# Kernel tuning notes

Measured on AMD Instinct MI355X. Metric: run time of the kernel, lower is better.

The kernel has to match this reference:

```python
import jax, jax.numpy as jnp
import numpy as np

B, N, DIM, QK_DIM, HEADS, GS, M = 4, 8000, 256, 128, 8, 128, 256


def setup_inputs() -> dict:
    key = jax.random.key(0)
    ks = jax.random.split(key, 8)
    normed_x = jax.random.normal(ks[0], (B, N, DIM), jnp.float32)
    # idx_last is a per-batch permutation (token reordering index), shape [B, N, 1]
    idx_last = jax.vmap(lambda k: jax.random.permutation(k, N))(
        jax.random.split(ks[1], B)).astype(jnp.int32)[..., None]
    k_global = jax.random.normal(ks[2], (HEADS, M, QK_DIM // HEADS), jnp.float32)
    v_global = jax.random.normal(ks[3], (HEADS, M, DIM // HEADS), jnp.float32)
    s = 1.0 / np.sqrt(DIM).astype(np.float32)
    Wq = jax.random.normal(ks[4], (QK_DIM, DIM), jnp.float32) * s
    Wk = jax.random.normal(ks[5], (QK_DIM, DIM), jnp.float32) * s
    Wv = jax.random.normal(ks[6], (DIM, DIM), jnp.float32) * s
    Wp = jax.random.normal(ks[7], (DIM, DIM), jnp.float32) * s
    return {"normed_x": normed_x, "idx_last": idx_last, "k_global": k_global,
            "v_global": v_global, "Wq": Wq, "Wk": Wk, "Wv": Wv, "Wp": Wp}


def _forward(normed_x, idx_last, k_global, v_global, Wq, Wk, Wv, Wp):
    x = normed_x
    b, n, _ = x.shape
    h = HEADS
    idx = idx_last[..., 0]  # [B, N]

    q = x @ Wq.T  # [B, N, QK_DIM]
    k = x @ Wk.T  # [B, N, QK_DIM]
    v = x @ Wv.T  # [B, N, DIM]

    # reorder tokens (gather along the token axis)
    q = jnp.take_along_axis(q, idx[:, :, None], axis=1)
    k = jnp.take_along_axis(k, idx[:, :, None], axis=1)
    v = jnp.take_along_axis(v, idx[:, :, None], axis=1)

    gs = min(n, GS)
    ng = (n + gs - 1) // gs
    pad_n = ng * gs - n

    # pad queries by reflecting the tail, then split into ng groups of gs
    pq = jnp.concatenate([q, jnp.flip(q[:, n - pad_n:n], axis=1)], axis=1)
    pq = pq.reshape(b, ng, gs, h, -1).transpose(0, 1, 3, 2, 4)  # b ng h gs dq

    # keys/values padded with an extra gs of reflected tail -> overlapping windows
    kr = jnp.concatenate([k, jnp.flip(k[:, n - pad_n - gs:n], axis=1)], axis=1)
    vr = jnp.concatenate([v, jnp.flip(v[:, n - pad_n - gs:n], axis=1)], axis=1)
    k_win = jnp.concatenate([kr[:, :ng * gs].reshape(b, ng, gs, -1),
                             kr[:, gs:].reshape(b, ng, gs, -1)], axis=2)
    v_win = jnp.concatenate([vr[:, :ng * gs].reshape(b, ng, gs, -1),
                             vr[:, gs:].reshape(b, ng, gs, -1)], axis=2)
    pk = k_win.reshape(b, ng, 2 * gs, h, -1).transpose(0, 1, 3, 2, 4)  # b ng h 2gs dq
    pv = v_win.reshape(b, ng, 2 * gs, h, -1).transpose(0, 1, 3, 2, 4)  # b ng h 2gs dv

    scale = pq.shape[-1] ** (-0.5)

    # local overlapping-window attention
    s1 = jnp.einsum('bghqd,bghkd->bghqk', pq, pk) * scale
    o1 = jnp.einsum('bghqk,bghkd->bghqd', jax.nn.softmax(s1, axis=-1), pv)

    # global attention (k_global/v_global broadcast over batch and groups)
    s2 = jnp.einsum('bghqd,hmd->bghqm', pq, k_global) * scale
    o2 = jnp.einsum('bghqm,hmd->bghqd', jax.nn.softmax(s2, axis=-1), v_global)

    out = (o1 + o2).transpose(0, 1, 3, 2, 4).reshape(b, ng * gs, -1)[:, :n]

    # scatter back to original token order: res[b, idx[b, i]] = out[b, i]
    b_idx = jnp.arange(b)[:, None]
    out = out.at[b_idx, idx].set(out)
    return out @ Wp.T


def reference(normed_x, idx_last, k_global, v_global, Wq, Wk, Wv, Wp):
    return _forward(normed_x, idx_last, k_global, v_global, Wq, Wk, Wv, Wp)
```

## Files before the change

kernel.cpp:

```cpp
#include <hip/hip_runtime.h>

typedef __attribute__((ext_vector_type(8))) short short8;
typedef __attribute__((ext_vector_type(4))) short short4v;
typedef __attribute__((ext_vector_type(4))) float f32x4;
typedef unsigned short ushort_t;

#define MFMA_BF16_K32(A,B,C) __builtin_amdgcn_mfma_f32_16x16x32_bf16(A,B,C,0,0,0)
#define MFMA_BF16_K16(A,B,C) __builtin_amdgcn_mfma_f32_16x16x16bf16_1k(A,B,C,0,0,0)

static constexpr int Bc  = 4;
static constexpr int Nn  = 8000;
static constexpr int N2  = 8192;
static constexpr int DIMc = 256;
static constexpr float SC2 = 0.36067376022224085f;

__device__ __forceinline__ unsigned short f2bf(float f){
  unsigned int u = __float_as_uint(f);
  u = (u + 0x7FFFu + ((u >> 16) & 1u)) >> 16;
  return (unsigned short)u;
}
__device__ __forceinline__ uint2 pack4(f32x4 v){
  uint2 r;
  r.x = (unsigned)f2bf(v[0]) | ((unsigned)f2bf(v[1]) << 16);
  r.y = (unsigned)f2bf(v[2]) | ((unsigned)f2bf(v[3]) << 16);
  return r;
}
__device__ __forceinline__ unsigned cvtpk(float lo, float hi){
  unsigned r;
  asm("v_cvt_pk_bf16_f32 %0, %1, %2" : "=v"(r) : "v"(lo), "v"(hi));
  return r;
}
__device__ __forceinline__ float rexp2(float x){
  float r;
  asm("v_exp_f32 %0, %1" : "=v"(r) : "v"(x));
  return r;
}
__device__ __forceinline__ float bfhi(unsigned u){ return __uint_as_float(u & 0xffff0000u); }
__device__ __forceinline__ float bflo(unsigned u){ return __uint_as_float(u << 16); }
__device__ __forceinline__ int vperm(int t){
  return (t & ~31) | (((t >> 2) & 3) * 8 + ((t >> 4) & 1) * 4 + (t & 3));
}

__global__ __launch_bounds__(256) void prep_kernel(
    const float* __restrict__ Wq, const float* __restrict__ Wk,
    const float* __restrict__ Wv, const float* __restrict__ Wp,
    const float* __restrict__ kg, const float* __restrict__ vg,
    ushort_t* __restrict__ Wcs, ushort_t* __restrict__ Wps,
    ushort_t* __restrict__ vgT, ushort_t* __restrict__ kgb)
{
  int i = blockIdx.x * 256 + threadIdx.x;
  if (i < 131072){
    int jj = i & 7, f = i >> 3;
    int l = f & 63, kc = (f >> 6) & 7, ctw = f >> 9;
    int col = ctw * 16 + (l & 15);
    int k   = kc * 32 + (l >> 4) * 8 + jj;
    float v;
    if (col < 128)      v = Wq[col * 256 + k] * SC2;
    else if (col < 256) v = Wk[(col - 128) * 256 + k];
    else                v = Wv[(col - 256) * 256 + k];
    Wcs[i] = f2bf(v);
  } else if (i < 196608){
    int o = i - 131072;
    int jj = o & 7, f = o >> 3;
    int l = f & 63, kc = (f >> 6) & 7, ctw = f >> 9;
    int col = ctw * 16 + (l & 15);
    int k   = kc * 32 + (l >> 4) * 8 + jj;
    Wps[o] = f2bf(Wp[col * 256 + k]);
  } else if (i < 262144){
    int o = i - 196608;
    int c = o & 31, m = (o >> 5) & 255, h = o >> 13;
    vgT[(h * 32 + c) * 256 + vperm(m)] = f2bf(vg[o]);
  } else {
    int j = i - 262144;
    kgb[j] = f2bf(kg[j]);
  }
}

__global__ __launch_bounds__(256) void proj_kernel(
    const float* __restrict__ X, const ushort_t* __restrict__ Wcs,
    const int* __restrict__ idx, ushort_t* __restrict__ qh,
    ushort_t* __restrict__ kh, ushort_t* __restrict__ vT)
{
  const int b  = blockIdx.y;
  const int r0 = blockIdx.x * 64;
  const int tid = threadIdx.x;
  const int w = tid >> 6, l = tid & 63, g4 = l >> 4, q16 = l & 15;
  __shared__ unsigned Xs[64][132];

  #pragma unroll
  for (int r = 0; r < 16; ++r){
    int row = r * 4 + w;
    int tok = idx[b * Nn + r0 + row];
    float4 xv = reinterpret_cast<const float4*>(X + (size_t)(b * Nn + tok) * DIMc)[l];
    uint2 u; u.x = cvtpk(xv.x, xv.y); u.y = cvtpk(xv.z, xv.w);
    *reinterpret_cast<uint2*>(&Xs[row][l * 2]) = u;
  }
  __syncthreads();

  f32x4 acc[4][8];
  #pragma unroll
  for (int mt = 0; mt < 4; ++mt)
    #pragma unroll
    for (int ct = 0; ct < 8; ++ct) acc[mt][ct] = f32x4{0.f, 0.f, 0.f, 0.f};
  #pragma unroll
  for (int kc = 0; kc < 8; ++kc){
    short8 a[4];
    #pragma unroll
    for (int mt = 0; mt < 4; ++mt){
      uint4 au = *reinterpret_cast<const uint4*>(&Xs[mt * 16 + q16][kc * 16 + g4 * 4]);
      a[mt] = __builtin_bit_cast(short8, au);
    }
    #pragma unroll
    for (int ct = 0; ct < 8; ++ct){
      short8 bb = *reinterpret_cast<const short8*>(
          Wcs + ((size_t)((w * 8 + ct) * 8 + kc) * 64 + l) * 8);
      #pragma unroll
      for (int mt = 0; mt < 4; ++mt) acc[mt][ct] = MFMA_BF16_K32(a[mt], bb, acc[mt][ct]);
    }
  }
  if (w < 2){
    ushort_t* dst = (w == 0) ? qh : kh;
    #pragma unroll
    for (int ct = 0; ct < 8; ++ct){
      #pragma unroll
      for (int mt = 0; mt < 4; ++mt){
        #pragma unroll
        for (int r = 0; r < 4; ++r){
          int j = r0 + mt * 16 + g4 * 4 + r;
          dst[((size_t)(b * 8 + ct) * N2 + j) * 16 + q16] = f2bf(acc[mt][ct][r]);
        }
      }
    }
  } else {
    #pragma unroll
    for (int ct = 0; ct < 8; ++ct){
      int col = (w - 2) * 128 + ct * 16 + q16;
      #pragma unroll
      for (int mt = 0; mt < 4; ++mt){
        int jb = r0 + (mt >> 1) * 32 + g4 * 8 + (mt & 1) * 4;
        *reinterpret_cast<uint2*>(vT + (size_t)(b * 256 + col) * N2 + jb) = pack4(acc[mt][ct]);
      }
    }
  }
}

__global__ __launch_bounds__(256) void reflect_fill_kernel(
    ushort_t* __restrict__ qh, ushort_t* __restrict__ kh, ushort_t* __restrict__ vT)
{
  int t = blockIdx.x * 256 + threadIdx.x;
  if (t < 24576){
    int e = t & 1;
    int r = (t >> 1) % 192;
    int p = (t >> 1) / 192;
    int b = p >> 4, q = p & 15;
    ushort_t* base = (q < 8) ? qh : kh;
    int h = q & 7;
    size_t plane = (size_t)(b * 8 + h) * N2 * 16;
    const uint4* src = reinterpret_cast<const uint4*>(base + plane + (size_t)(7999 - r) * 16);
    uint4*       dst = reinterpret_cast<uint4*>(base + plane + (size_t)(8000 + r) * 16);
    dst[e] = src[e];
  } else {
    int u = t - 24576;
    int r = u / 192, i2 = u % 192;
    vT[(size_t)r * N2 + vperm(8000 + i2)] = vT[(size_t)r * N2 + vperm(7999 - i2)];
  }
}

__global__ __launch_bounds__(256) void attn_kernel(
    const ushort_t* __restrict__ qh, const ushort_t* __restrict__ kh,
    const ushort_t* __restrict__ vT,
    const ushort_t* __restrict__ kg, const ushort_t* __restrict__ vgT,
    ushort_t* __restrict__ aoh)
{
  const int go = blockIdx.x, hp = blockIdx.y, b = blockIdx.z;
  const int tid = threadIdx.x;
  const int w = tid >> 6, l = tid & 63, g4 = l >> 4, q16 = l & 15;
  const int h = hp * 4 + w;
  __shared__ unsigned Pex[4][8][16][17];
  const f32x4 z4 = {0.f, 0.f, 0.f, 0.f};
  const size_t bh = (size_t)(b * 8 + h);
  const ushort_t* Kloc = kh + (bh * N2 + go * 128) * 16;
  const ushort_t* Vloc = vT + (size_t)(b * 256 + h * 32) * N2 + go * 128;
  const ushort_t* Kg   = kg + (size_t)h * 256 * 16;
  const ushort_t* Vg   = vgT + (size_t)h * 32 * 256;
  const ushort_t* Qb   = qh + (bh * N2 + go * 128) * 16;
  ushort_t*       Ob   = aoh + (bh * N2 + go * 128) * 32;

  short8 ones;
  #pragma unroll
  for (int j = 0; j < 8; ++j) ones[j] = (short)0x3F80;

  #pragma unroll 1
  for (int pass = 0; pass < 2; ++pass){
    const ushort_t* kbase = (pass == 0) ? Kloc : Kg;
    short4v karr[16];
    #pragma unroll
    for (int t = 0; t < 16; ++t)
      karr[t] = *reinterpret_cast<const short4v*>(
          kbase + (size_t)(t * 16 + q16) * 16 + g4 * 4);
    const ushort_t* v0;
    size_t rstride;
    if (pass == 0){ v0 = Vloc + (size_t)q16 * N2 + g4 * 8;  rstride = (size_t)16 * N2; }
    else          { v0 = Vg   + (size_t)q16 * 256 + g4 * 8; rstride = (size_t)16 * 256; }
    uint4 va[8], vb[8];
    #pragma unroll
    for (int t2 = 0; t2 < 8; ++t2){
      va[t2] = *reinterpret_cast<const uint4*>(v0 + t2 * 32);
      vb[t2] = *reinterpret_cast<const uint4*>(v0 + rstride + t2 * 32);
    }

    #pragma unroll 2
    for (int qt = 0; qt < 8; ++qt){
      short4v qf = *reinterpret_cast<const short4v*>(
          Qb + (size_t)(qt * 16 + q16) * 16 + g4 * 4);
      f32x4 s[16];
      __builtin_amdgcn_s_setprio(1);
      #pragma unroll
      for (int t = 0; t < 16; ++t) s[t] = MFMA_BF16_K16(karr[t], qf, z4);
      __builtin_amdgcn_s_setprio(0);
      uint4 p4[8];
      #pragma unroll
      for (int t2 = 0; t2 < 8; ++t2){
        float e0 = rexp2(s[2*t2][0]);
        float e1 = rexp2(s[2*t2][1]);
        float e2 = rexp2(s[2*t2][2]);
        float e3 = rexp2(s[2*t2][3]);
        float f0 = rexp2(s[2*t2+1][0]);
        float f1 = rexp2(s[2*t2+1][1]);
        float f2 = rexp2(s[2*t2+1][2]);
        float f3 = rexp2(s[2*t2+1][3]);
        p4[t2].x = cvtpk(e0, e1); p4[t2].y = cvtpk(e2, e3);
        p4[t2].z = cvtpk(f0, f1); p4[t2].w = cvtpk(f2, f3);
      }
      f32x4 o0 = z4, o1 = z4, dacc = z4;
      __builtin_amdgcn_s_setprio(1);
      #pragma unroll
      for (int t2 = 0; t2 < 8; ++t2){
        short8 pf = __builtin_bit_cast(short8, p4[t2]);
        o0   = MFMA_BF16_K32(__builtin_bit_cast(short8, va[t2]), pf, o0);
        o1   = MFMA_BF16_K32(__builtin_bit_cast(short8, vb[t2]), pf, o1);
        dacc = MFMA_BF16_K32(ones, pf, dacc);
      }
      __builtin_amdgcn_s_setprio(0);
      float invd = 1.0f / dacc[0];
      unsigned* pb = &Pex[w][qt][q16][0];
      if (pass == 0){
        pb[g4 * 2]         = cvtpk(o0[0] * invd, o0[1] * invd);
        pb[g4 * 2 + 1]     = cvtpk(o0[2] * invd, o0[3] * invd);
        pb[8 + g4 * 2]     = cvtpk(o1[0] * invd, o1[1] * invd);
        pb[8 + g4 * 2 + 1] = cvtpk(o1[2] * invd, o1[3] * invd);
      } else {
        unsigned u0 = pb[g4 * 2],     u1 = pb[g4 * 2 + 1];
        unsigned u2 = pb[8 + g4 * 2], u3 = pb[8 + g4 * 2 + 1];
        f32x4 r0, r1;
        r0[0] = __builtin_fmaf(o0[0], invd, bflo(u0));
        r0[1] = __builtin_fmaf(o0[1], invd, bfhi(u0));
        r0[2] = __builtin_fmaf(o0[2], invd, bflo(u1));
        r0[3] = __builtin_fmaf(o0[3], invd, bfhi(u1));
        r1[0] = __builtin_fmaf(o1[0], invd, bflo(u2));
        r1[1] = __builtin_fmaf(o1[1], invd, bfhi(u2));
        r1[2] = __builtin_fmaf(o1[2], invd, bflo(u3));
        r1[3] = __builtin_fmaf(o1[3], invd, bfhi(u3));
        uint2 s0, s1;
        s0.x = cvtpk(r0[0], r0[1]); s0.y = cvtpk(r0[2], r0[3]);
        s1.x = cvtpk(r1[0], r1[1]); s1.y = cvtpk(r1[2], r1[3]);
        size_t base = (size_t)(qt * 16 + q16) * 32;
        *reinterpret_cast<uint2*>(Ob + base + g4 * 4)      = s0;
        *reinterpret_cast<uint2*>(Ob + base + 16 + g4 * 4) = s1;
      }
    }
  }
}

__global__ __launch_bounds__(256) void final_kernel(
    const ushort_t* __restrict__ A, const ushort_t* __restrict__ Wps,
    const int* __restrict__ idx, float* __restrict__ out)
{
  const int b  = blockIdx.y;
  const int r0 = blockIdx.x * 64;
  const int tid = threadIdx.x;
  const int w = tid >> 6, l = tid & 63, g4 = l >> 4, q16 = l & 15;
  f32x4 acc[4][4];
  #pragma unroll
  for (int mt = 0; mt < 4; ++mt)
    #pragma unroll
    for (int ct = 0; ct < 4; ++ct) acc[mt][ct] = f32x4{0.f, 0.f, 0.f, 0.f};
  #pragma unroll
  for (int kc = 0; kc < 8; ++kc){
    short8 a[4];
    #pragma unroll
    for (int mt = 0; mt < 4; ++mt)
      a[mt] = *reinterpret_cast<const short8*>(
          A + ((size_t)(b * 8 + kc) * N2 + r0 + mt * 16 + q16) * 32 + g4 * 8);
    #pragma unroll
    for (int ct = 0; ct < 4; ++ct){
      short8 bb = *reinterpret_cast<const short8*>(
          Wps + ((size_t)((w * 4 + ct) * 8 + kc) * 64 + l) * 8);
      #pragma unroll
      for (int mt = 0; mt < 4; ++mt) acc[mt][ct] = MFMA_BF16_K32(a[mt], bb, acc[mt][ct]);
    }
  }
  #pragma unroll
  for (int mt = 0; mt < 4; ++mt){
    int orow[4];
    #pragma unroll
    for (int r = 0; r < 4; ++r) orow[r] = idx[b * Nn + r0 + mt * 16 + g4 * 4 + r];
    #pragma unroll
    for (int ct = 0; ct < 4; ++ct){
      int col = w * 64 + ct * 16 + q16;
      #pragma unroll
      for (int r = 0; r < 4; ++r)
        out[(size_t)(b * Nn + orow[r]) * DIMc + col] = acc[mt][ct][r];
    }
  }
}

extern "C" void kernel_launch(void* const* d_in, const int* in_sizes, int n_in,
                              void* d_out, int out_size, void* d_ws, size_t ws_size,
                              hipStream_t stream)
{
  const float* x   = (const float*)d_in[0];
  const int*   idx = (const int*)d_in[1];
  const float* kg  = (const float*)d_in[2];
  const float* vg  = (const float*)d_in[3];
  const float* Wq  = (const float*)d_in[4];
  const float* Wk  = (const float*)d_in[5];
  const float* Wv  = (const float*)d_in[6];
  const float* Wp  = (const float*)d_in[7];
  float* out = (float*)d_out;

  char* ws = (char*)d_ws;
  size_t off = 0;
  auto alloc = [&](size_t bytes) -> void* {
    void* p = ws + off; off += (bytes + 255) & ~(size_t)255; return p;
  };
  ushort_t* qh   = (ushort_t*)alloc((size_t)Bc * 8 * N2 * 16 * 2);
  ushort_t* kh   = (ushort_t*)alloc((size_t)Bc * 8 * N2 * 16 * 2);
  ushort_t* vT   = (ushort_t*)alloc((size_t)Bc * 256 * N2 * 2);
  ushort_t* aoh  = (ushort_t*)alloc((size_t)Bc * 8 * N2 * 32 * 2);
  ushort_t* Wcs  = (ushort_t*)alloc((size_t)512 * 256 * 2);
  ushort_t* Wps  = (ushort_t*)alloc((size_t)256 * 256 * 2);
  ushort_t* vgT  = (ushort_t*)alloc((size_t)8 * 32 * 256 * 2);
  ushort_t* kgb  = (ushort_t*)alloc((size_t)8 * 256 * 16 * 2);

  hipLaunchKernelGGL(prep_kernel,  dim3(1152), dim3(256), 0, stream,
                     Wq, Wk, Wv, Wp, kg, vg, Wcs, Wps, vgT, kgb);
  hipLaunchKernelGGL(proj_kernel,  dim3(125, 4), dim3(256), 0, stream, x, Wcs, idx, qh, kh, vT);
  hipLaunchKernelGGL(reflect_fill_kernel, dim3(864), dim3(256), 0, stream, qh, kh, vT);
  hipLaunchKernelGGL(attn_kernel,  dim3(63, 2, 4), dim3(256), 0, stream, qh, kh, vT, kgb, vgT, aoh);
  hipLaunchKernelGGL(final_kernel, dim3(125, 4), dim3(256), 0, stream, aoh, Wps, idx, out);
}
```

Measured before the change: 97.08 us.

## Split local and global attention passes across waves, sum in projection GEMM

Each wave now handles only one head and one attention pass (local window or global keys) instead of running both passes sequentially. The grid's head dimension doubles to keep coverage, and the LDS exchange buffer is removed. The two partial outputs go to separate workspace buffers, and the final projection kernel adds them by issuing two MFMAs per tile (o1·Wp + o2·Wp). This doubles parallelism and removes the serial dependency inside attention. In exchange it doubles attention-output memory traffic and the MFMA count in the final GEMM.

```diff
diff --git a/kernel.cpp b/kernel.cpp
--- a/kernel.cpp
+++ b/kernel.cpp
@@ -35,8 +35,6 @@
   asm("v_exp_f32 %0, %1" : "=v"(r) : "v"(x));
   return r;
 }
-__device__ __forceinline__ float bfhi(unsigned u){ return __uint_as_float(u & 0xffff0000u); }
-__device__ __forceinline__ float bflo(unsigned u){ return __uint_as_float(u << 16); }
 __device__ __forceinline__ int vperm(int t){
   return (t & ~31) | (((t >> 2) & 3) * 8 + ((t >> 4) & 1) * 4 + (t & 3));
 }
@@ -170,110 +168,93 @@
     const ushort_t* __restrict__ qh, const ushort_t* __restrict__ kh,
     const ushort_t* __restrict__ vT,
     const ushort_t* __restrict__ kg, const ushort_t* __restrict__ vgT,
-    ushort_t* __restrict__ aoh)
+    ushort_t* __restrict__ aoh0, ushort_t* __restrict__ aoh1)
 {
   const int go = blockIdx.x, hp = blockIdx.y, b = blockIdx.z;
   const int tid = threadIdx.x;
   const int w = tid >> 6, l = tid & 63, g4 = l >> 4, q16 = l & 15;
-  const int h = hp * 4 + w;
-  __shared__ unsigned Pex[4][8][16][17];
+  const int h = hp * 2 + (w >> 1);
+  const int pass = w & 1;
   const f32x4 z4 = {0.f, 0.f, 0.f, 0.f};
   const size_t bh = (size_t)(b * 8 + h);
-  const ushort_t* Kloc = kh + (bh * N2 + go * 128) * 16;
-  const ushort_t* Vloc = vT + (size_t)(b * 256 + h * 32) * N2 + go * 128;
-  const ushort_t* Kg   = kg + (size_t)h * 256 * 16;
-  const ushort_t* Vg   = vgT + (size_t)h * 32 * 256;
-  const ushort_t* Qb   = qh + (bh * N2 + go * 128) * 16;
-  ushort_t*       Ob   = aoh + (bh * N2 + go * 128) * 32;
+  const ushort_t* Qb = qh + (bh * N2 + go * 128) * 16;
+  ushort_t*       Ob = (pass ? aoh1 : aoh0) + (bh * N2 + go * 128) * 32;
 
   short8 ones;
   #pragma unroll
   for (int j = 0; j < 8; ++j) ones[j] = (short)0x3F80;
 
-  #pragma unroll 1
-  for (int pass = 0; pass < 2; ++pass){
-    const ushort_t* kbase = (pass == 0) ? Kloc : Kg;
-    short4v karr[16];
-    #pragma unroll
-    for (int t = 0; t < 16; ++t)
-      karr[t] = *reinterpret_cast<const short4v*>(
-          kbase + (size_t)(t * 16 + q16) * 16 + g4 * 4);
-    const ushort_t* v0;
-    size_t rstride;
-    if (pass == 0){ v0 = Vloc + (size_t)q16 * N2 + g4 * 8;  rstride = (size_t)16 * N2; }
-    else          { v0 = Vg   + (size_t)q16 * 256 + g4 * 8; rstride = (size_t)16 * 256; }
-    uint4 va[8], vb[8];
+  const ushort_t* kbase = pass ? (kg + (size_t)h * 256 * 16)
+                               : (kh + (bh * N2 + go * 128) * 16);
+  short4v karr[16];
+  #pragma unroll
+  for (int t = 0; t < 16; ++t)
+    karr[t] = *reinterpret_cast<const short4v*>(
+        kbase + (size_t)(t * 16 + q16) * 16 + g4 * 4);
+  const ushort_t* v0;
+  size_t rstride;
+  if (!pass){
+    v0 = vT + (size_t)(b * 256 + h * 32) * N2 + go * 128 + (size_t)q16 * N2 + g4 * 8;
+    rstride = (size_t)16 * N2;
+  } else {
+    v0 = vgT + (size_t)h * 32 * 256 + (size_t)q16 * 256 + g4 * 8;
+    rstride = (size_t)16 * 256;
+  }
+  uint4 va[8], vb[8];
+  #pragma unroll
+  for (int t2 = 0; t2 < 8; ++t2){
+    va[t2] = *reinterpret_cast<const uint4*>(v0 + t2 * 32);
+    vb[t2] = *reinterpret_cast<const uint4*>(v0 + rstride + t2 * 32);
+  }
+
+  #pragma unroll 2
+  for (int qt = 0; qt < 8; ++qt){
+    short4v qf = *reinterpret_cast<const short4v*>(
+        Qb + (size_t)(qt * 16 + q16) * 16 + g4 * 4);
+    f32x4 s[16];
+    __builtin_amdgcn_s_setprio(1);
+    #pragma unroll
+    for (int t = 0; t < 16; ++t) s[t] = MFMA_BF16_K16(karr[t], qf, z4);
+    __builtin_amdgcn_s_setprio(0);
+    uint4 p4[8];
     #pragma unroll
     for (int t2 = 0; t2 < 8; ++t2){
-      va[t2] = *reinterpret_cast<const uint4*>(v0 + t2 * 32);
-      vb[t2] = *reinterpret_cast<const uint4*>(v0 + rstride + t2 * 32);
-    }
-
-    #pragma unroll 2
-    for (int qt = 0; qt < 8; ++qt){
-      short4v qf = *reinterpret_cast<const short4v*>(
-          Qb + (size_t)(qt * 16 + q16) * 16 + g4 * 4);
-      f32x4 s[16];
-      __builtin_amdgcn_s_setprio(1);
-      #pragma unroll
-      for (int t = 0; t < 16; ++t) s[t] = MFMA_BF16_K16(karr[t], qf, z4);
-      __builtin_amdgcn_s_setprio(0);
-      uint4 p4[8];
-      #pragma unroll
-      for (int t2 = 0; t2 < 8; ++t2){
-        float e0 = rexp2(s[2*t2][0]);
-        float e1 = rexp2(s[2*t2][1]);
-        float e2 = rexp2(s[2*t2][2]);
-        float e3 = rexp2(s[2*t2][3]);
-        float f0 = rexp2(s[2*t2+1][0]);
-        float f1 = rexp2(s[2*t2+1][1]);
-        float f2 = rexp2(s[2*t2+1][2]);
-        float f3 = rexp2(s[2*t2+1][3]);
-        p4[t2].x = cvtpk(e0, e1); p4[t2].y = cvtpk(e2, e3);
-        p4[t2].z = cvtpk(f0, f1); p4[t2].w = cvtpk(f2, f3);
-      }
-      f32x4 o0 = z4, o1 = z4, dacc = z4;
-      __builtin_amdgcn_s_setprio(1);
-      #pragma unroll
-      for (int t2 = 0; t2 < 8; ++t2){
-        short8 pf = __builtin_bit_cast(short8, p4[t2]);
-        o0   = MFMA_BF16_K32(__builtin_bit_cast(short8, va[t2]), pf, o0);
-        o1   = MFMA_BF16_K32(__builtin_bit_cast(short8, vb[t2]), pf, o1);
-        dacc = MFMA_BF16_K32(ones, pf, dacc);
-      }
-      __builtin_amdgcn_s_setprio(0);
-      float invd = 1.0f / dacc[0];
-      unsigned* pb = &Pex[w][qt][q16][0];
-      if (pass == 0){
-        pb[g4 * 2]         = cvtpk(o0[0] * invd, o0[1] * invd);
-        pb[g4 * 2 + 1]     = cvtpk(o0[2] * invd, o0[3] * invd);
-        pb[8 + g4 * 2]     = cvtpk(o1[0] * invd, o1[1] * invd);
-        pb[8 + g4 * 2 + 1] = cvtpk(o1[2] * invd, o1[3] * invd);
-      } else {
-        unsigned u0 = pb[g4 * 2],     u1 = pb[g4 * 2 + 1];
-        unsigned u2 = pb[8 + g4 * 2], u3 = pb[8 + g4 * 2 + 1];
-        f32x4 r0, r1;
-        r0[0] = __builtin_fmaf(o0[0], invd, bflo(u0));
-        r0[1] = __builtin_fmaf(o0[1], invd, bfhi(u0));
-        r0[2] = __builtin_fmaf(o0[2], invd, bflo(u1));
-        r0[3] = __builtin_fmaf(o0[3], invd, bfhi(u1));
-        r1[0] = __builtin_fmaf(o1[0], invd, bflo(u2));
-        r1[1] = __builtin_fmaf(o1[1], invd, bfhi(u2));
-        r1[2] = __builtin_fmaf(o1[2], invd, bflo(u3));
-        r1[3] = __builtin_fmaf(o1[3], invd, bfhi(u3));
-        uint2 s0, s1;
-        s0.x = cvtpk(r0[0], r0[1]); s0.y = cvtpk(r0[2], r0[3]);
-        s1.x = cvtpk(r1[0], r1[1]); s1.y = cvtpk(r1[2], r1[3]);
-        size_t base = (size_t)(qt * 16 + q16) * 32;
-        *reinterpret_cast<uint2*>(Ob + base + g4 * 4)      = s0;
-        *reinterpret_cast<uint2*>(Ob + base + 16 + g4 * 4) = s1;
-      }
-    }
+      float e0 = rexp2(s[2*t2][0]);
+      float e1 = rexp2(s[2*t2][1]);
+      float e2 = rexp2(s[2*t2][2]);
+      float e3 = rexp2(s[2*t2][3]);
+      float f0 = rexp2(s[2*t2+1][0]);
+      float f1 = rexp2(s[2*t2+1][1]);
+      float f2 = rexp2(s[2*t2+1][2]);
+      float f3 = rexp2(s[2*t2+1][3]);
+      p4[t2].x = cvtpk(e0, e1); p4[t2].y = cvtpk(e2, e3);
+      p4[t2].z = cvtpk(f0, f1); p4[t2].w = cvtpk(f2, f3);
+    }
+    f32x4 o0 = z4, o1 = z4, dacc = z4;
+    __builtin_amdgcn_s_setprio(1);
+    #pragma unroll
+    for (int t2 = 0; t2 < 8; ++t2){
+      short8 pf = __builtin_bit_cast(short8, p4[t2]);
+      o0   = MFMA_BF16_K32(__builtin_bit_cast(short8, va[t2]), pf, o0);
+      o1   = MFMA_BF16_K32(__builtin_bit_cast(short8, vb[t2]), pf, o1);
+      dacc = MFMA_BF16_K32(ones, pf, dacc);
+    }
+    __builtin_amdgcn_s_setprio(0);
+    float invd = 1.0f / dacc[0];
+    uint2 s0, s1;
+    s0.x = cvtpk(o0[0] * invd, o0[1] * invd);
+    s0.y = cvtpk(o0[2] * invd, o0[3] * invd);
+    s1.x = cvtpk(o1[0] * invd, o1[1] * invd);
+    s1.y = cvtpk(o1[2] * invd, o1[3] * invd);
+    size_t base = (size_t)(qt * 16 + q16) * 32;
+    *reinterpret_cast<uint2*>(Ob + base + g4 * 4)      = s0;
+    *reinterpret_cast<uint2*>(Ob + base + 16 + g4 * 4) = s1;
   }
 }
 
 __global__ __launch_bounds__(256) void final_kernel(
-    const ushort_t* __restrict__ A, const ushort_t* __restrict__ Wps,
+    const ushort_t* __restrict__ A0, const ushort_t* __restrict__ A1,
+    const ushort_t* __restrict__ Wps,
     const int* __restrict__ idx, float* __restrict__ out)
 {
   const int b  = blockIdx.y;
@@ -287,17 +268,22 @@
     for (int ct = 0; ct < 4; ++ct) acc[mt][ct] = f32x4{0.f, 0.f, 0.f, 0.f};
   #pragma unroll
   for (int kc = 0; kc < 8; ++kc){
-    short8 a[4];
-    #pragma unroll
-    for (int mt = 0; mt < 4; ++mt)
-      a[mt] = *reinterpret_cast<const short8*>(
-          A + ((size_t)(b * 8 + kc) * N2 + r0 + mt * 16 + q16) * 32 + g4 * 8);
+    short8 a0[4], a1[4];
+    #pragma unroll
+    for (int mt = 0; mt < 4; ++mt){
+      size_t off = ((size_t)(b * 8 + kc) * N2 + r0 + mt * 16 + q16) * 32 + g4 * 8;
+      a0[mt] = *reinterpret_cast<const short8*>(A0 + off);
+      a1[mt] = *reinterpret_cast<const short8*>(A1 + off);
+    }
     #pragma unroll
     for (int ct = 0; ct < 4; ++ct){
       short8 bb = *reinterpret_cast<const short8*>(
           Wps + ((size_t)((w * 4 + ct) * 8 + kc) * 64 + l) * 8);
       #pragma unroll
-      for (int mt = 0; mt < 4; ++mt) acc[mt][ct] = MFMA_BF16_K32(a[mt], bb, acc[mt][ct]);
+      for (int mt = 0; mt < 4; ++mt){
+        acc[mt][ct] = MFMA_BF16_K32(a0[mt], bb, acc[mt][ct]);
+        acc[mt][ct] = MFMA_BF16_K32(a1[mt], bb, acc[mt][ct]);
+      }
     }
   }
   #pragma unroll
@@ -337,7 +323,8 @@
   ushort_t* qh   = (ushort_t*)alloc((size_t)Bc * 8 * N2 * 16 * 2);
   ushort_t* kh   = (ushort_t*)alloc((size_t)Bc * 8 * N2 * 16 * 2);
   ushort_t* vT   = (ushort_t*)alloc((size_t)Bc * 256 * N2 * 2);
-  ushort_t* aoh  = (ushort_t*)alloc((size_t)Bc * 8 * N2 * 32 * 2);
+  ushort_t* aoh0 = (ushort_t*)alloc((size_t)Bc * 8 * N2 * 32 * 2);
+  ushort_t* aoh1 = (ushort_t*)alloc((size_t)Bc * 8 * N2 * 32 * 2);
   ushort_t* Wcs  = (ushort_t*)alloc((size_t)512 * 256 * 2);
   ushort_t* Wps  = (ushort_t*)alloc((size_t)256 * 256 * 2);
   ushort_t* vgT  = (ushort_t*)alloc((size_t)8 * 32 * 256 * 2);
@@ -347,6 +334,7 @@
                      Wq, Wk, Wv, Wp, kg, vg, Wcs, Wps, vgT, kgb);
   hipLaunchKernelGGL(proj_kernel,  dim3(125, 4), dim3(256), 0, stream, x, Wcs, idx, qh, kh, vT);
   hipLaunchKernelGGL(reflect_fill_kernel, dim3(864), dim3(256), 0, stream, qh, kh, vT);
-  hipLaunchKernelGGL(attn_kernel,  dim3(63, 2, 4), dim3(256), 0, stream, qh, kh, vT, kgb, vgT, aoh);
-  hipLaunchKernelGGL(final_kernel, dim3(125, 4), dim3(256), 0, stream, aoh, Wps, idx, out);
-}
+  hipLaunchKernelGGL(attn_kernel,  dim3(63, 4, 4), dim3(256), 0, stream,
+                     qh, kh, vT, kgb, vgT, aoh0, aoh1);
+  hipLaunchKernelGGL(final_kernel, dim3(125, 4), dim3(256), 0, stream, aoh0, aoh1, Wps, idx, out);
+}
```

Result: no change. 95.66 us (median of 3 runs) (-1.5%).
